# Performance work log

Measured on AMD Instinct MI355X. Metric: run time of the kernel, lower is better.

Reference implementation:

```python
import jax, jax.numpy as jnp
import numpy as np

N_NODES = 50000
N_EDGES = 800000
N_ATOMS = 100
HID = 128
N_LAYERS = 3
OUT_LAYERS = 2
OUT_DIM = 1
N_GRAPHS = 1024
EPS = 1e-12  # F.normalize eps


def setup_inputs() -> dict:
    key = jax.random.key(0)
    ks = jax.random.split(key, 12)
    s = 0.05
    x_ori = jax.random.randint(ks[0], (N_NODES,), 0, N_ATOMS)
    edge_index = jax.random.randint(ks[1], (2, N_EDGES), 0, N_NODES)
    edge_attr = jax.random.normal(ks[2], (N_EDGES, 1), jnp.float32)
    batch_ids = jnp.sort(jax.random.randint(ks[3], (N_NODES,), 0, N_GRAPHS))
    embd_w = jax.random.normal(ks[4], (N_ATOMS, HID), jnp.float32) * s
    gamma_w = jnp.ones((N_LAYERS, N_ATOMS, 1), jnp.float32)  # reset_parameters sets ones
    w_atom_W = jax.random.normal(ks[5], (N_LAYERS, HID, HID), jnp.float32) * s
    w_atom_b = jax.random.normal(ks[6], (N_LAYERS, HID), jnp.float32) * s
    lin_W = jax.random.normal(ks[7], (OUT_LAYERS, HID, HID), jnp.float32) * s
    lin_b = jax.random.normal(ks[8], (OUT_LAYERS, HID), jnp.float32) * s
    wp_W = jax.random.normal(ks[9], (HID, OUT_DIM), jnp.float32) * s
    wp_b = jax.random.normal(ks[10], (OUT_DIM,), jnp.float32) * s
    return dict(x_ori=x_ori, edge_index=edge_index, edge_attr=edge_attr,
                batch_ids=batch_ids, embd_w=embd_w, gamma_w=gamma_w,
                w_atom_W=w_atom_W, w_atom_b=w_atom_b, lin_W=lin_W, lin_b=lin_b,
                wp_W=wp_W, wp_b=wp_b)


def reference(x_ori, edge_index, edge_attr, batch_ids, embd_w, gamma_w,
              w_atom_W, w_atom_b, lin_W, lin_b, wp_W, wp_b):
    src, dst = edge_index[0], edge_index[1]
    x = embd_w[x_ori]  # [N, H]
    for l in range(N_LAYERS):
        h = jax.nn.relu(x @ w_atom_W[l] + w_atom_b[l])            # [N, H]
        gam = jax.nn.sigmoid(gamma_w[l])[x_ori][dst]              # [E, 1]
        ew = jnp.exp(-gam * edge_attr ** 2)                       # [E, 1]
        msg = ew * h[src]                                         # [E, H] gather+weight
        agg = jax.ops.segment_sum(msg, dst, num_segments=N_NODES) # scatter-add
        y = agg + x
        nrm = jnp.maximum(jnp.linalg.norm(y, axis=1, keepdims=True), EPS)
        x = y / nrm                                               # F.normalize(., 2, 1)
    for i in range(OUT_LAYERS):
        x = jax.nn.relu(x @ lin_W[i] + lin_b[i])
    m_x = jax.ops.segment_sum(x, batch_ids, num_segments=N_GRAPHS)  # [G, H]
    props = m_x @ wp_W + wp_b                                      # [G, 1]
    return jnp.squeeze(props, axis=1)                              # [G]
```

## Files before the change

### kernel.cpp

```cpp
#include <hip/hip_runtime.h>
#include <hip/hip_bf16.h>
#include <math.h>

typedef __hip_bfloat16 bf16;
typedef unsigned int uint;
typedef unsigned short ushort;
typedef __attribute__((ext_vector_type(8))) short short8;
typedef __attribute__((ext_vector_type(4))) float f32x4;

#define HID 128
#define NN 50000
#define NE 800000
#define NG 1024
#define NA 100
#define CAP 64

#define NB   98
#define RCAP 10240

__device__ __forceinline__ uint bf16_rne_hi(float f) {
    uint u = __float_as_uint(f);
    return (u + 0x7fffu + ((u >> 16) & 1u)) & 0xffff0000u;
}
__device__ __forceinline__ uint pack_bf16x2(float lo, float hi) {
    return (bf16_rne_hi(lo) >> 16) | bf16_rne_hi(hi);
}
__device__ __forceinline__ ushort bf16_rne(float f) {
    uint u = __float_as_uint(f);
    return (ushort)((u + 0x7fffu + ((u >> 16) & 1u)) >> 16);
}
__device__ __forceinline__ float lof(uint u) { return __uint_as_float(u << 16); }
__device__ __forceinline__ float hif(uint u) { return __uint_as_float(u & 0xffff0000u); }
__device__ __forceinline__ float load_f(const void* p, int i, int f32) {
    return f32 ? ((const float*)p)[i]
               : __uint_as_float((uint)((const ushort*)p)[i] << 16);
}
__device__ __forceinline__ int detect_f32(const void* emb) {
    const ushort* p = (const ushort*)emb;
    int lane = threadIdx.x & 63;
    float v = __uint_as_float((uint)p[lane * 4] << 16);
    int bad0 = (!(v == v) || fabsf(v) > 1e4f || (v != 0.0f && fabsf(v) < 1e-10f));
    float w = __uint_as_float((uint)p[lane * 4 + 2] << 16);
    int bad1 = (!(w == w) || fabsf(w) > 1e4f || (w != 0.0f && fabsf(w) < 1e-10f));
    int cnt = __popcll(__ballot(bad0)) + __popcll(__ballot(bad1));
    return cnt > 16;
}

#define A_BLKS     196
#define EMB_BLKS   ((NN * 64) / 256)
#define PACKW_BLKS (5 * 16384 / 256)
#define CVT_CNT    (300 + 384 + 256 + 128 + 1)
#define CVT_BLKS   5
#define PR_B1      A_BLKS
#define PR_B2      (PR_B1 + EMB_BLKS)
#define PR_B3      (PR_B2 + PACKW_BLKS)
#define PR_B4      (PR_B3 + CVT_BLKS)
#define PR_B5      (PR_B4 + 4)
#define PREP_GRID  (PR_B5 + 1)

__global__ void prep_k(const int* __restrict__ xo, const void* __restrict__ emb,
                       const void* __restrict__ gamw, const void* __restrict__ wAW,
                       const void* __restrict__ wAb, const void* __restrict__ linW,
                       const void* __restrict__ linb, const void* __restrict__ wpW,
                       const void* __restrict__ wpb,
                       const int* __restrict__ esrc, const int* __restrict__ edst,
                       const void* __restrict__ ea,
                       uint* __restrict__ xb, ushort* __restrict__ Wp,
                       float* __restrict__ f_sgam, float* __restrict__ f_wAb,
                       float* __restrict__ f_linb, float* __restrict__ f_wp,
                       float* __restrict__ f_wpb,
                       uint2* __restrict__ rec, int* __restrict__ bcur,
                       float* __restrict__ gpn,
                       float* __restrict__ grf, int* __restrict__ flag) {
    int f32 = detect_f32(emb);
    int b = blockIdx.x, t = threadIdx.x;
    if (b < PR_B1) {
        __shared__ int hist[NB];
        __shared__ int obase[NB];
        if (t < NB) hist[t] = 0;
        __syncthreads();
        int  dv[16];
        uint rv[16];
#pragma unroll
        for (int k = 0; k < 4; ++k) {
            int e = b * 4096 + k * 1024 + t * 4;
            if (e + 3 < NE) {
                int4 s4 = *(const int4*)(esrc + e);
                int4 d4 = *(const int4*)(edst + e);
                float a0, a1, a2, a3;
                if (f32) {
                    float4 f = *(const float4*)((const float*)ea + e);
                    a0 = f.x; a1 = f.y; a2 = f.z; a3 = f.w;
                } else {
                    ushort4 u = *(const ushort4*)((const ushort*)ea + e);
                    a0 = __uint_as_float((uint)u.x << 16);
                    a1 = __uint_as_float((uint)u.y << 16);
                    a2 = __uint_as_float((uint)u.z << 16);
                    a3 = __uint_as_float((uint)u.w << 16);
                }
                atomicAdd(&hist[d4.x >> 9], 1);
                atomicAdd(&hist[d4.y >> 9], 1);
                atomicAdd(&hist[d4.z >> 9], 1);
                atomicAdd(&hist[d4.w >> 9], 1);
                dv[k * 4 + 0] = d4.x; rv[k * 4 + 0] = (uint)(s4.x & 0xffff) | ((uint)bf16_rne(a0 * a0) << 16);
                dv[k * 4 + 1] = d4.y; rv[k * 4 + 1] = (uint)(s4.y & 0xffff) | ((uint)bf16_rne(a1 * a1) << 16);
                dv[k * 4 + 2] = d4.z; rv[k * 4 + 2] = (uint)(s4.z & 0xffff) | ((uint)bf16_rne(a2 * a2) << 16);
                dv[k * 4 + 3] = d4.w; rv[k * 4 + 3] = (uint)(s4.w & 0xffff) | ((uint)bf16_rne(a3 * a3) << 16);
            } else {
                dv[k * 4 + 0] = dv[k * 4 + 1] = dv[k * 4 + 2] = dv[k * 4 + 3] = -1;
                rv[k * 4 + 0] = rv[k * 4 + 1] = rv[k * 4 + 2] = rv[k * 4 + 3] = 0;
            }
        }
        __syncthreads();
        if (t < NB) {
            int c = hist[t];
            obase[t] = c ? atomicAdd(&bcur[t], c) : 0;
            hist[t] = 0;
        }
        __syncthreads();
#pragma unroll
        for (int k = 0; k < 16; ++k) {
            int d = dv[k];
            if (d >= 0) {
                int bb = d >> 9;
                int r = atomicAdd(&hist[bb], 1);
                int idx = obase[bb] + r;
                if (idx < RCAP) rec[bb * RCAP + idx] = make_uint2(rv[k], (uint)d);
            }
        }
    } else if (b < PR_B2) {
        int gidx = (b - PR_B1) * 256 + t;
        int node = gidx >> 6, c2 = gidx & 63;
        int xon = xo[node];
        int base = xon * HID + c2 * 2;
        xb[gidx] = pack_bf16x2(load_f(emb, base, f32), load_f(emb, base + 1, f32));
        if (c2 < 3) {
            float v = load_f(gamw, c2 * 100 + xon, f32);
            gpn[c2 * NN + node] = 1.0f / (1.0f + __expf(-v));
        }
    } else if (b < PR_B3) {
        int t2 = (b - PR_B2) * 256 + t;
        int i   = t2 & 7;
        int n   = (t2 >> 3) & 15;
        int q   = (t2 >> 7) & 3;
        int j16 = (t2 >> 9) & 7;
        int ks  = (t2 >> 12) & 3;
        int mat = t2 >> 14;
        int k = ks * 32 + q * 8 + i;
        int j = j16 * 16 + n;
        const void* W = (mat < 3) ? wAW : linW;
        int off = ((mat < 3) ? mat : (mat - 3)) * 16384 + k * HID + j;
        Wp[t2] = bf16_rne(load_f(W, off, f32));
    } else if (b < PR_B4) {
        int idx = (b - PR_B3) * 256 + t;
        if (idx < 300) {
            float v = load_f(gamw, idx, f32);
            f_sgam[idx] = 1.0f / (1.0f + __expf(-v));
        } else if (idx < 684) {
            f_wAb[idx - 300] = load_f(wAb, idx - 300, f32);
        } else if (idx < 940) {
            f_linb[idx - 684] = load_f(linb, idx - 684, f32);
        } else if (idx < 1068) {
            f_wp[idx - 940] = load_f(wpW, idx - 940, f32);
        } else if (idx < CVT_CNT) {
            f_wpb[0] = load_f(wpb, 0, f32);
        }
    } else if (b < PR_B5) {
        grf[(b - PR_B4) * 256 + t] = 0.0f;
    } else {
        if (t == 0) *flag = f32;
    }
}

__device__ __forceinline__ void gemm_core(const uint* __restrict__ xb,
                                          const ushort* __restrict__ Wp,
                                          const float* __restrict__ bias,
                                          int m0, int lane,
                                          f32x4 acc0[8], f32x4 acc1[8]) {
    int ln15 = lane & 15;
    int q    = lane >> 4;
    int mA = min(m0 + ln15, NN - 1);
    int mB = min(m0 + 16 + ln15, NN - 1);
    const short8* A8 = (const short8*)xb;
    const short8* B8 = (const short8*)Wp;
#pragma unroll
    for (int j16 = 0; j16 < 8; ++j16) {
        float bv = bias[j16 * 16 + ln15];
        acc0[j16] = (f32x4){bv, bv, bv, bv};
        acc1[j16] = acc0[j16];
    }
#pragma unroll
    for (int ks = 0; ks < 4; ++ks) {
        short8 a0 = A8[mA * 16 + ks * 4 + q];
        short8 a1 = A8[mB * 16 + ks * 4 + q];
#pragma unroll
        for (int j16 = 0; j16 < 8; ++j16) {
            short8 b = B8[(ks * 8 + j16) * 64 + q * 16 + ln15];
            acc0[j16] = __builtin_amdgcn_mfma_f32_16x16x32_bf16(a0, b, acc0[j16], 0, 0, 0);
            acc1[j16] = __builtin_amdgcn_mfma_f32_16x16x32_bf16(a1, b, acc1[j16], 0, 0, 0);
        }
    }
}

__device__ __forceinline__ void gemm_store(f32x4 acc0[8], f32x4 acc1[8],
                                           int m0, int lane, uint* __restrict__ outb) {
    int ln15 = lane & 15;
    int q    = lane >> 4;
    ushort* ob = (ushort*)outb;
#pragma unroll
    for (int reg = 0; reg < 4; ++reg) {
        int n0 = m0 + q * 4 + reg;
        int n1 = n0 + 16;
#pragma unroll
        for (int j16 = 0; j16 < 8; ++j16) {
            if (n0 < NN)
                ob[(size_t)n0 * HID + j16 * 16 + ln15] = bf16_rne(fmaxf(acc0[j16][reg], 0.0f));
            if (n1 < NN)
                ob[(size_t)n1 * HID + j16 * 16 + ln15] = bf16_rne(fmaxf(acc1[j16][reg], 0.0f));
        }
    }
}

#define G1_BLKS ((NN + 255) / 256)
__global__ __launch_bounds__(512) void work2_k(const uint* __restrict__ xb,
                                               const ushort* __restrict__ Wp,
                                               const float* __restrict__ bias,
                                               uint* __restrict__ outb,
                                               const uint2* __restrict__ rec,
                                               const int* __restrict__ bcur,
                                               uint* __restrict__ csr,
                                               int* __restrict__ degarr) {
    int b = blockIdx.x, t = threadIdx.x;
    if (b < NB) {
        __shared__ int ldeg[512];
        ldeg[t] = 0;
        __syncthreads();
        int cnt = min(bcur[b], RCAP);
        int nb0 = b << 9;
        for (int i = t; i < cnt; i += 512) {
            uint2 r = rec[b * RCAP + i];
            int dst = (int)r.y;
            int p = atomicAdd(&ldeg[dst - nb0], 1);
            if (p < CAP) csr[dst * CAP + p] = r.x;
        }
        __syncthreads();
        int n = nb0 + t;
        if (n < NN) degarr[n] = min(ldeg[t], CAP);
    } else {
        f32x4 acc0[8], acc1[8];
        int m0 = (b - NB) * 256 + (t >> 6) * 32;
        gemm_core(xb, Wp, bias, m0, t & 63, acc0, acc1);
        gemm_store(acc0, acc1, m0, t & 63, outb);
    }
}

template<int LAST>
__global__ __launch_bounds__(512) void gg_k(const int* __restrict__ degarr,
                                            const uint* __restrict__ csr,
                                            const float* __restrict__ gpn,
                                            const uint* __restrict__ hb_in,
                                            uint* __restrict__ xb,
                                            const ushort* __restrict__ Wp,
                                            const float* __restrict__ bias,
                                            uint* __restrict__ hb_out,
                                            const ushort* __restrict__ Wp2,
                                            const float* __restrict__ bias2,
                                            const float* __restrict__ wp,
                                            const int* __restrict__ batch,
                                            float* __restrict__ grf) {
    __shared__ uint  lds_a[2048];
    __shared__ uint  lds_b[LAST ? 2048 : 1];
    __shared__ float lds_p[LAST ? 256 : 1];
    int t = threadIdx.x;
    int w = t >> 6, lane = t & 63;
    int q = lane >> 4, ln15 = lane & 15;
    int n0 = blockIdx.x * 32;

    int j  = w * 4 + q;
    int n  = n0 + j;
    int nc = min(n, NN - 1);
    int deg = (n < NN) ? degarr[n] : 0;
    const uint* cp = csr + (size_t)nc * CAP;
    float g = gpn[nc];
    uint4 xv = *(const uint4*)(xb + (size_t)nc * 64 + ln15 * 4);
    float ax0 = 0.f, ax1 = 0.f, ax2 = 0.f, ax3 = 0.f;
    float ay0 = 0.f, ay1 = 0.f, ay2 = 0.f, ay3 = 0.f;
    uint4 c4 = *(const uint4*)(cp);
    for (int e = 0; e < deg; e += 4) {
        uint4 c4n = *(const uint4*)(cp + e + 4);
        uint cc[4] = {c4.x, c4.y, c4.z, c4.w};
#pragma unroll
        for (int i = 0; i < 4; ++i) {
            bool vld = (e + i) < deg;
            float wi = vld ? __expf(-g * hif(cc[i])) : 0.0f;
            int   ri = vld ? (int)(cc[i] & 0xffffu) : 0;
            uint4 v  = *(const uint4*)(hb_in + (size_t)ri * 64 + ln15 * 4);
            ax0 = fmaf(wi, lof(v.x), ax0); ay0 = fmaf(wi, hif(v.x), ay0);
            ax1 = fmaf(wi, lof(v.y), ax1); ay1 = fmaf(wi, hif(v.y), ay1);
            ax2 = fmaf(wi, lof(v.z), ax2); ay2 = fmaf(wi, hif(v.z), ay2);
            ax3 = fmaf(wi, lof(v.w), ax3); ay3 = fmaf(wi, hif(v.w), ay3);
        }
        c4 = c4n;
    }
    {
        float yx0 = ax0 + lof(xv.x), yy0 = ay0 + hif(xv.x);
        float yx1 = ax1 + lof(xv.y), yy1 = ay1 + hif(xv.y);
        float yx2 = ax2 + lof(xv.z), yy2 = ay2 + hif(xv.z);
        float yx3 = ax3 + lof(xv.w), yy3 = ay3 + hif(xv.w);
        float ss = yx0 * yx0 + yy0 * yy0 + yx1 * yx1 + yy1 * yy1
                 + yx2 * yx2 + yy2 * yy2 + yx3 * yx3 + yy3 * yy3;
        ss += __shfl_xor(ss, 1); ss += __shfl_xor(ss, 2);
        ss += __shfl_xor(ss, 4); ss += __shfl_xor(ss, 8);
        float inv = 1.0f / fmaxf(sqrtf(ss), 1e-12f);
        uint4 o;
        o.x = pack_bf16x2(yx0 * inv, yy0 * inv);
        o.y = pack_bf16x2(yx1 * inv, yy1 * inv);
        o.z = pack_bf16x2(yx2 * inv, yy2 * inv);
        o.w = pack_bf16x2(yx3 * inv, yy3 * inv);
        if (!LAST && n < NN) *(uint4*)(xb + (size_t)n * 64 + ln15 * 4) = o;
        int rt = j >> 4, m = j & 15;
        *(uint4*)&lds_a[(((rt * 4 + (ln15 >> 2)) * 64) + (ln15 & 3) * 16 + m) * 4] = o;
    }
    __syncthreads();

    const short8* A8 = (const short8*)lds_a;
    const short8* B8 = (const short8*)Wp;
    f32x4 acc[2];
    {
        float bv = bias[w * 16 + ln15];
        acc[0] = (f32x4){bv, bv, bv, bv};
        acc[1] = acc[0];
    }
#pragma unroll
    for (int ks = 0; ks < 4; ++ks) {
        short8 b = B8[(ks * 8 + w) * 64 + lane];
#pragma unroll
        for (int rt = 0; rt < 2; ++rt) {
            short8 a = A8[(rt * 4 + ks) * 64 + lane];
            acc[rt] = __builtin_amdgcn_mfma_f32_16x16x32_bf16(a, b, acc[rt], 0, 0, 0);
        }
    }
    if (!LAST) {
        ushort* ob = (ushort*)hb_out;
#pragma unroll
        for (int rt = 0; rt < 2; ++rt) {
#pragma unroll
            for (int reg = 0; reg < 4; ++reg) {
                int nn = n0 + rt * 16 + q * 4 + reg;
                if (nn < NN)
                    ob[(size_t)nn * HID + w * 16 + ln15] = bf16_rne(fmaxf(acc[rt][reg], 0.0f));
            }
        }
    } else {
        ushort* sb = (ushort*)lds_b;
        int c  = w * 16 + ln15;
        int c2 = c >> 1, cb = c2 & 3, cq = (c2 >> 2) & 3, cks = c2 >> 4, lohi = c & 1;
#pragma unroll
        for (int rt = 0; rt < 2; ++rt) {
#pragma unroll
            for (int reg = 0; reg < 4; ++reg) {
                int m = q * 4 + reg;
                int uidx = ((rt * 4 + cks) * 64 + cq * 16 + m) * 4 + cb;
                sb[uidx * 2 + lohi] = bf16_rne(fmaxf(acc[rt][reg], 0.0f));
            }
        }
        __syncthreads();
        const short8* A8b = (const short8*)lds_b;
        const short8* B8b = (const short8*)Wp2;
        f32x4 acc3[2];
        {
            float bv = bias2[w * 16 + ln15];
            acc3[0] = (f32x4){bv, bv, bv, bv};
            acc3[1] = acc3[0];
        }
#pragma unroll
        for (int ks = 0; ks < 4; ++ks) {
            short8 bb = B8b[(ks * 8 + w) * 64 + lane];
#pragma unroll
            for (int rt = 0; rt < 2; ++rt) {
                short8 a = A8b[(rt * 4 + ks) * 64 + lane];
                acc3[rt] = __builtin_amdgcn_mfma_f32_16x16x32_bf16(a, bb, acc3[rt], 0, 0, 0);
            }
        }
        float wv = wp[w * 16 + ln15];
#pragma unroll
        for (int rt = 0; rt < 2; ++rt) {
#pragma unroll
            for (int reg = 0; reg < 4; ++reg) {
                float p = fmaxf(acc3[rt][reg], 0.0f) * wv;
                p += __shfl_xor(p, 1); p += __shfl_xor(p, 2);
                p += __shfl_xor(p, 4); p += __shfl_xor(p, 8);
                if (ln15 == 0) lds_p[(rt * 16 + q * 4 + reg) * 8 + w] = p;
            }
        }
        __syncthreads();
        if (t < 32) {
            float sm = 0.0f;
#pragma unroll
            for (int k = 0; k < 8; ++k) sm += lds_p[t * 8 + k];
            int nn = n0 + t;
            if (nn < NN) atomicAdd(&grf[batch[nn]], sm);
        }
    }
}

__global__ void out_k(const float* __restrict__ grf, const float* __restrict__ wpb,
                      void* __restrict__ out, const int* __restrict__ flag) {
    int g = blockIdx.x * 256 + threadIdx.x;
    if (g >= NG) return;
    float r = grf[g] + wpb[0];
    if (*flag) ((float*)out)[g] = r;
    else       ((bf16*)out)[g] = __float2bfloat16(r);
}

extern "C" void kernel_launch(void* const* d_in, const int* in_sizes, int n_in,
                              void* d_out, int out_size, void* d_ws, size_t ws_size,
                              hipStream_t stream) {
    const int*  xo    = (const int*)d_in[0];
    const int*  ei    = (const int*)d_in[1];
    const int*  src   = ei;
    const int*  dst   = ei + NE;
    const void* ea    = d_in[2];
    const int*  batch = (const int*)d_in[3];
    const void* emb   = d_in[4];
    const void* gamw  = d_in[5];
    const void* wAW   = d_in[6];
    const void* wAb   = d_in[7];
    const void* linW  = d_in[8];
    const void* linb  = d_in[9];
    const void* wpW   = d_in[10];
    const void* wpb   = d_in[11];

    uint*  xb     = (uint*)d_ws;
    uint*  hA     = xb + (size_t)NN * 64;
    uint*  hB     = hA + (size_t)NN * 64;
    uint2* rec    = (uint2*)hB;
    uint*  csr    = hB + (size_t)NN * 64;
    int*   degarr = (int*)(csr + (size_t)NN * CAP);
    float* grf    = (float*)(degarr + NN);
    float* P      = grf + NG;
    float* f_sgam = P;
    float* f_wAb  = f_sgam + 304;
    float* f_linb = f_wAb + 384;
    float* f_wp   = f_linb + 256;
    float* f_wpb  = f_wp + 128;
    int*   flag   = (int*)(f_wpb + 8);
    ushort* Wp    = (ushort*)(flag + 8);
    int*   bcur   = (int*)(Wp + 5 * 16384);
    float* gpn    = (float*)(bcur + 128);

    hipMemsetAsync(bcur, 0, NB * sizeof(int), stream);

    prep_k<<<PREP_GRID, 256, 0, stream>>>(xo, emb, gamw, wAW, wAb, linW, linb, wpW, wpb,
                                          src, dst, ea,
                                          xb, Wp, f_sgam, f_wAb, f_linb, f_wp, f_wpb,
                                          rec, bcur, gpn, grf, flag);

    work2_k<<<NB + G1_BLKS, 512, 0, stream>>>(xb, Wp, f_wAb, hA, rec, bcur, csr, degarr);

    const int GG_GRID = (NN + 31) / 32;
    gg_k<0><<<GG_GRID, 512, 0, stream>>>(degarr, csr, gpn,          hA, xb,
                                         Wp + 1 * 16384, f_wAb + 128, hB,
                                         nullptr, nullptr, nullptr, nullptr, nullptr);
    gg_k<0><<<GG_GRID, 512, 0, stream>>>(degarr, csr, gpn + NN,     hB, xb,
                                         Wp + 2 * 16384, f_wAb + 256, hA,
                                         nullptr, nullptr, nullptr, nullptr, nullptr);
    gg_k<1><<<GG_GRID, 512, 0, stream>>>(degarr, csr, gpn + 2 * NN, hA, xb,
                                         Wp + 3 * 16384, f_linb,      nullptr,
                                         Wp + 4 * 16384, f_linb + HID, f_wp, batch, grf);

    out_k<<<(NG + 255) / 256, 256, 0, stream>>>(grf, f_wpb, d_out, flag);
}
```

Measured before the change: 265.2 us.

## Split gather-aggregate into separate kernel with per-edge-slot lane parallelism

Moves the neighbor gather and weighted sum out of the fused layer kernel into a dedicated kernel where each wave handles one node, with four lane groups taking different edges and column quarters split across blocks. The result is reduced by shuffles and written as bf16 to a new aggregate buffer, which the renamed normalize+GEMM kernel then reads. The intent is more memory-level parallelism and better occupancy for the irregular gather. In exchange it adds three extra launches, a round trip of the aggregate through global memory, and an extra bf16 rounding of the aggregate.

```diff
diff --git a/kernel.cpp b/kernel.cpp
--- a/kernel.cpp
+++ b/kernel.cpp
@@ -254,11 +254,42 @@
     }
 }
 
+#define GQ_GRID ((NN / 8 / 2) * 8)
+__global__ __launch_bounds__(512) void gq_k(const int* __restrict__ degarr,
+                                            const uint* __restrict__ csr,
+                                            const float* __restrict__ gpnl,
+                                            const uint* __restrict__ hb_in,
+                                            uint* __restrict__ aggb) {
+    int t = threadIdx.x, w = t >> 6, lane = t & 63;
+    int slot4 = lane >> 4, l15 = lane & 15;
+    int b = blockIdx.x, pair = b >> 3, slot = b & 7;
+    int qt   = slot & 3;
+    int tile = pair * 2 + (slot >> 2);
+    int n = tile * 8 + w;
+    int cu = qt * 16 + l15;
+    int deg = degarr[n];
+    const uint* cp = csr + (size_t)n * CAP;
+    float g = gpnl[n];
+    float ax = 0.0f, ay = 0.0f;
+    uint cc = __builtin_nontemporal_load(cp + slot4);
+    for (int e = 0; e < deg; e += 4) {
+        uint cn = __builtin_nontemporal_load(cp + e + 4 + slot4);
+        bool vld = (e + slot4) < deg;
+        float wi = vld ? __expf(-g * hif(cc)) : 0.0f;
+        int   ri = vld ? (int)(cc & 0xffffu) : 0;
+        uint  v  = hb_in[(size_t)ri * 64 + cu];
+        ax = fmaf(wi, lof(v), ax);
+        ay = fmaf(wi, hif(v), ay);
+        cc = cn;
+    }
+    ax += __shfl_xor(ax, 16); ax += __shfl_xor(ax, 32);
+    ay += __shfl_xor(ay, 16); ay += __shfl_xor(ay, 32);
+    if (slot4 == 0)
+        __builtin_nontemporal_store(pack_bf16x2(ax, ay), &aggb[(size_t)n * 64 + cu]);
+}
+
 template<int LAST>
-__global__ __launch_bounds__(512) void gg_k(const int* __restrict__ degarr,
-                                            const uint* __restrict__ csr,
-                                            const float* __restrict__ gpn,
-                                            const uint* __restrict__ hb_in,
+__global__ __launch_bounds__(512) void ng_k(const uint* __restrict__ aggb,
                                             uint* __restrict__ xb,
                                             const ushort* __restrict__ Wp,
                                             const float* __restrict__ bias,
@@ -276,37 +307,16 @@
     int q = lane >> 4, ln15 = lane & 15;
     int n0 = blockIdx.x * 32;
 
-    int j  = w * 4 + q;
-    int n  = n0 + j;
-    int nc = min(n, NN - 1);
-    int deg = (n < NN) ? degarr[n] : 0;
-    const uint* cp = csr + (size_t)nc * CAP;
-    float g = gpn[nc];
-    uint4 xv = *(const uint4*)(xb + (size_t)nc * 64 + ln15 * 4);
-    float ax0 = 0.f, ax1 = 0.f, ax2 = 0.f, ax3 = 0.f;
-    float ay0 = 0.f, ay1 = 0.f, ay2 = 0.f, ay3 = 0.f;
-    uint4 c4 = *(const uint4*)(cp);
-    for (int e = 0; e < deg; e += 4) {
-        uint4 c4n = *(const uint4*)(cp + e + 4);
-        uint cc[4] = {c4.x, c4.y, c4.z, c4.w};
-#pragma unroll
-        for (int i = 0; i < 4; ++i) {
-            bool vld = (e + i) < deg;
-            float wi = vld ? __expf(-g * hif(cc[i])) : 0.0f;
-            int   ri = vld ? (int)(cc[i] & 0xffffu) : 0;
-            uint4 v  = *(const uint4*)(hb_in + (size_t)ri * 64 + ln15 * 4);
-            ax0 = fmaf(wi, lof(v.x), ax0); ay0 = fmaf(wi, hif(v.x), ay0);
-            ax1 = fmaf(wi, lof(v.y), ax1); ay1 = fmaf(wi, hif(v.y), ay1);
-            ax2 = fmaf(wi, lof(v.z), ax2); ay2 = fmaf(wi, hif(v.z), ay2);
-            ax3 = fmaf(wi, lof(v.w), ax3); ay3 = fmaf(wi, hif(v.w), ay3);
-        }
-        c4 = c4n;
-    }
     {
-        float yx0 = ax0 + lof(xv.x), yy0 = ay0 + hif(xv.x);
-        float yx1 = ax1 + lof(xv.y), yy1 = ay1 + hif(xv.y);
-        float yx2 = ax2 + lof(xv.z), yy2 = ay2 + hif(xv.z);
-        float yx3 = ax3 + lof(xv.w), yy3 = ay3 + hif(xv.w);
+        int j  = w * 4 + q;
+        int n  = n0 + j;
+        int nc = min(n, NN - 1);
+        uint4 av = *(const uint4*)(aggb + (size_t)nc * 64 + ln15 * 4);
+        uint4 xv = *(const uint4*)(xb   + (size_t)nc * 64 + ln15 * 4);
+        float yx0 = lof(av.x) + lof(xv.x), yy0 = hif(av.x) + hif(xv.x);
+        float yx1 = lof(av.y) + lof(xv.y), yy1 = hif(av.y) + hif(xv.y);
+        float yx2 = lof(av.z) + lof(xv.z), yy2 = hif(av.z) + hif(xv.z);
+        float yx3 = lof(av.w) + lof(xv.w), yy3 = hif(av.w) + hif(xv.w);
         float ss = yx0 * yx0 + yy0 * yy0 + yx1 * yx1 + yy1 * yy1
                  + yx2 * yx2 + yy2 * yy2 + yx3 * yx3 + yy3 * yy3;
         ss += __shfl_xor(ss, 1); ss += __shfl_xor(ss, 2);
@@ -448,6 +458,7 @@
     ushort* Wp    = (ushort*)(flag + 8);
     int*   bcur   = (int*)(Wp + 5 * 16384);
     float* gpn    = (float*)(bcur + 128);
+    uint*  aggb   = (uint*)(gpn + 3 * NN);
 
     hipMemsetAsync(bcur, 0, NB * sizeof(int), stream);
 
@@ -459,14 +470,14 @@
     work2_k<<<NB + G1_BLKS, 512, 0, stream>>>(xb, Wp, f_wAb, hA, rec, bcur, csr, degarr);
 
     const int GG_GRID = (NN + 31) / 32;
-    gg_k<0><<<GG_GRID, 512, 0, stream>>>(degarr, csr, gpn,          hA, xb,
-                                         Wp + 1 * 16384, f_wAb + 128, hB,
+    gq_k<<<GQ_GRID, 512, 0, stream>>>(degarr, csr, gpn,          hA, aggb);
+    ng_k<0><<<GG_GRID, 512, 0, stream>>>(aggb, xb, Wp + 1 * 16384, f_wAb + 128, hB,
                                          nullptr, nullptr, nullptr, nullptr, nullptr);
-    gg_k<0><<<GG_GRID, 512, 0, stream>>>(degarr, csr, gpn + NN,     hB, xb,
-                                         Wp + 2 * 16384, f_wAb + 256, hA,
+    gq_k<<<GQ_GRID, 512, 0, stream>>>(degarr, csr, gpn + NN,     hB, aggb);
+    ng_k<0><<<GG_GRID, 512, 0, stream>>>(aggb, xb, Wp + 2 * 16384, f_wAb + 256, hA,
                                          nullptr, nullptr, nullptr, nullptr, nullptr);
-    gg_k<1><<<GG_GRID, 512, 0, stream>>>(degarr, csr, gpn + 2 * NN, hA, xb,
-                                         Wp + 3 * 16384, f_linb,      nullptr,
+    gq_k<<<GQ_GRID, 512, 0, stream>>>(degarr, csr, gpn + 2 * NN, hA, aggb);
+    ng_k<1><<<GG_GRID, 512, 0, stream>>>(aggb, xb, Wp + 3 * 16384, f_linb, nullptr,
                                          Wp + 4 * 16384, f_linb + HID, f_wp, batch, grf);
 
     out_k<<<(NG + 255) / 256, 256, 0, stream>>>(grf, f_wpb, d_out, flag);
```

Result: slower. 589.9 us (+122.5%).
